# Performance work log

Measured on AMD Instinct MI355X. Metric: run time of the kernel, lower is better.

## Reference

```python
import jax, jax.numpy as jnp
import numpy as np


def _side(x, y, W, w):
    # x: [B, Lx, d] attends over y: [B, Ly, d]
    alpha = jnp.einsum('bld,de->ble', x, W)          # bilinear projection
    alpha = jnp.einsum('ble,bme->blm', alpha, y)     # [B, Lx, Ly]
    alpha = jax.nn.softmax(alpha, axis=1)            # Keras softmax axis=1 (over Lx)
    a = jnp.einsum('blm,bmd->bld', alpha, y)         # attended context [B, Lx, d]
    out = jnp.concatenate([x - a, x * a], axis=-1)   # [B, Lx, 2d]
    beta = jax.nn.softmax(jnp.einsum('ble,eo->blo', out, w)[..., 0], axis=-1)  # [B, Lx]
    return jnp.einsum('bl,ble->be', beta, out)       # pooled [B, 2d]


def setup_inputs() -> dict:
    key = jax.random.key(0)
    k1, k2, k3, k4 = jax.random.split(key, 4)
    B, L, d = 512, 256, 512
    return {
        'i': jax.random.normal(k1, (B, L, d), dtype=jnp.float32),
        'j': jax.random.normal(k2, (B, L, d), dtype=jnp.float32),
        'W': jax.random.normal(k3, (d, d), dtype=jnp.float32) * 0.05,
        'w': jax.random.normal(k4, (2 * d, 1), dtype=jnp.float32) * 0.05,
    }


def reference(i, j, W, w):
    out_i = _side(i, j, W, w)
    out_j = _side(j, i, W, w)
    return (out_i, out_j)
```

## Files before the change

kernel.cpp:

```cpp
#include <hip/hip_runtime.h>

#define LL 256
#define DD 512

typedef _Float16 f16;
typedef _Float16 f16x4_t __attribute__((ext_vector_type(4)));
typedef _Float16 f16x8_t __attribute__((ext_vector_type(8)));
typedef float f32x4_t __attribute__((ext_vector_type(4)));

__device__ __forceinline__ char* swzp(char* base, unsigned row, unsigned byte) {
  return base + (byte ^ ((row & 7u) << 4));
}
__device__ __forceinline__ const char* swzp(const char* base, unsigned row, unsigned byte) {
  return base + (byte ^ ((row & 7u) << 4));
}

__global__ void k_prep(const float* __restrict__ W, f16* __restrict__ Wt) {
  __shared__ float t[64][65];
  int bx = blockIdx.x & 7;
  int by = blockIdx.x >> 3;
  int tx = threadIdx.x & 63, tg = threadIdx.x >> 6;
  for (int r = tg; r < 64; r += 4)
    t[r][tx] = W[(by * 64 + r) * DD + bx * 64 + tx];
  __syncthreads();
  for (int r = tg; r < 64; r += 4)
    Wt[(bx * 64 + r) * DD + by * 64 + tx] = (f16)t[tx][r];
}

struct Smem {
  f16 A_w[256 * 256];
  union {
    struct { f16 bufX[256 * 32]; f16 bufW[128 * 32]; } p0;
    struct { f16 bufP[256 * 32]; f16 bufY[64 * 32]; } pa;
    f16 yT[128 * 64];
  } st;
  float colred[4][64];
  float colmax[64];
  float colinv[64];
  float gp[2][256];
  float beta[256];
};

__global__ __launch_bounds__(512, 2)
void k_main(const float* __restrict__ gi, const float* __restrict__ gj,
            const f16* __restrict__ Wt, const float* __restrict__ wv,
            f16* __restrict__ slabs, float* __restrict__ out) {
  __shared__ Smem sm;
  const int tid = threadIdx.x;
  const int lane = tid & 63;
  const int wave = tid >> 6;
  const int wm = wave & 3, wn = wave >> 2;
  const int lq = lane & 15, lg = lane >> 4;
  const int bid = blockIdx.x;
  const int b = bid >> 1, side = bid & 1;
  const float* __restrict__ x = (side ? gj : gi) + (size_t)b * (LL * DD);
  const float* __restrict__ y = (side ? gi : gj) + (size_t)b * (LL * DD);
  f16* __restrict__ slab = slabs + (size_t)bid * (LL * DD);

  char* const AW = (char*)sm.A_w;
  char* const BX = (char*)sm.st.p0.bufX;
  char* const BW = (char*)sm.st.p0.bufW;
  char* const BP = (char*)sm.st.pa.bufP;
  char* const BY = (char*)sm.st.pa.bufY;
  char* const YT = (char*)sm.st.yT;

  for (int nt = 0; nt < 4; ++nt) {
    f32x4_t acc[4][4];
#pragma unroll
    for (int mf = 0; mf < 4; ++mf)
#pragma unroll
      for (int nf = 0; nf < 4; ++nf)
        acc[mf][nf] = (f32x4_t){0.f, 0.f, 0.f, 0.f};

    for (int kt = 0; kt < 16; ++kt) {
#pragma unroll
      for (int c = tid; c < 1024; c += 512) {
        int row = c >> 2, sl = c & 3;
        const float* src = x + row * DD + kt * 32 + sl * 8;
        float4 a0 = *(const float4*)src;
        float4 a1 = *(const float4*)(src + 4);
        f16x8_t v;
        v[0] = (f16)a0.x; v[1] = (f16)a0.y; v[2] = (f16)a0.z; v[3] = (f16)a0.w;
        v[4] = (f16)a1.x; v[5] = (f16)a1.y; v[6] = (f16)a1.z; v[7] = (f16)a1.w;
        *(f16x8_t*)swzp(BX, row, row * 64u + sl * 16u) = v;
      }
      {
        int row = tid >> 2, sl = tid & 3;
        f16x8_t v = *(const f16x8_t*)(Wt + (nt * 128 + row) * DD + kt * 32 + sl * 8);
        *(f16x8_t*)swzp(BW, row, row * 64u + sl * 16u) = v;
      }
      __syncthreads();
      f16x8_t af[4], bf[4];
#pragma unroll
      for (int mf = 0; mf < 4; ++mf) {
        int row = wm * 64 + mf * 16 + lq;
        af[mf] = *(const f16x8_t*)swzp(BX, row, row * 64u + lg * 16u);
      }
#pragma unroll
      for (int nf = 0; nf < 4; ++nf) {
        int er = wn * 64 + nf * 16 + lq;
        bf[nf] = *(const f16x8_t*)swzp(BW, er, er * 64u + lg * 16u);
      }
#pragma unroll
      for (int mf = 0; mf < 4; ++mf)
#pragma unroll
        for (int nf = 0; nf < 4; ++nf)
          acc[mf][nf] = __builtin_amdgcn_mfma_f32_16x16x32_f16(af[mf], bf[nf], acc[mf][nf], 0, 0, 0);
      __syncthreads();
    }
#pragma unroll
    for (int mf = 0; mf < 4; ++mf)
#pragma unroll
      for (int nf = 0; nf < 4; ++nf)
#pragma unroll
        for (int r = 0; r < 4; ++r) {
          int row = wm * 64 + mf * 16 + lg * 4 + r;
          int col = nt * 128 + wn * 64 + nf * 16 + lq;
          slab[row * DD + col] = (f16)acc[mf][nf][r];
        }
  }
  __threadfence_block();
  __syncthreads();

  for (int mt = 0; mt < 4; ++mt) {
    f32x4_t acc[4][2];
#pragma unroll
    for (int mf = 0; mf < 4; ++mf)
#pragma unroll
      for (int nf = 0; nf < 2; ++nf)
        acc[mf][nf] = (f32x4_t){0.f, 0.f, 0.f, 0.f};

    for (int kt = 0; kt < 16; ++kt) {
#pragma unroll
      for (int c = tid; c < 1024; c += 512) {
        int row = c >> 2, sl = c & 3;
        f16x8_t v = *(const f16x8_t*)(slab + row * DD + kt * 32 + sl * 8);
        *(f16x8_t*)swzp(BP, row, row * 64u + sl * 16u) = v;
      }
      if (tid < 256) {
        int row = tid >> 2, sl = tid & 3;
        const float* src = y + (mt * 64 + row) * DD + kt * 32 + sl * 8;
        float4 a0 = *(const float4*)src;
        float4 a1 = *(const float4*)(src + 4);
        f16x8_t v;
        v[0] = (f16)a0.x; v[1] = (f16)a0.y; v[2] = (f16)a0.z; v[3] = (f16)a0.w;
        v[4] = (f16)a1.x; v[5] = (f16)a1.y; v[6] = (f16)a1.z; v[7] = (f16)a1.w;
        *(f16x8_t*)swzp(BY, row, row * 64u + sl * 16u) = v;
      }
      __syncthreads();
      f16x8_t af[4], bf[2];
#pragma unroll
      for (int mf = 0; mf < 4; ++mf) {
        int row = wm * 64 + mf * 16 + lq;
        af[mf] = *(const f16x8_t*)swzp(BP, row, row * 64u + lg * 16u);
      }
#pragma unroll
      for (int nf = 0; nf < 2; ++nf) {
        int mr = wn * 32 + nf * 16 + lq;
        bf[nf] = *(const f16x8_t*)swzp(BY, mr, mr * 64u + lg * 16u);
      }
#pragma unroll
      for (int mf = 0; mf < 4; ++mf)
#pragma unroll
        for (int nf = 0; nf < 2; ++nf)
          acc[mf][nf] = __builtin_amdgcn_mfma_f32_16x16x32_f16(af[mf], bf[nf], acc[mf][nf], 0, 0, 0);
      __syncthreads();
    }

    float vm[2];
#pragma unroll
    for (int nf = 0; nf < 2; ++nf) {
      float v = -3.4e38f;
#pragma unroll
      for (int mf = 0; mf < 4; ++mf)
#pragma unroll
        for (int r = 0; r < 4; ++r) v = fmaxf(v, acc[mf][nf][r]);
      v = fmaxf(v, __shfl_xor(v, 16));
      v = fmaxf(v, __shfl_xor(v, 32));
      vm[nf] = v;
    }
    if (lane < 16) {
      sm.colred[wm][wn * 32 + lane] = vm[0];
      sm.colred[wm][wn * 32 + 16 + lane] = vm[1];
    }
    __syncthreads();
    if (tid < 64)
      sm.colmax[tid] = fmaxf(fmaxf(sm.colred[0][tid], sm.colred[1][tid]),
                             fmaxf(sm.colred[2][tid], sm.colred[3][tid]));
    __syncthreads();
#pragma unroll
    for (int nf = 0; nf < 2; ++nf) {
      float cm = sm.colmax[wn * 32 + nf * 16 + lq];
      float s = 0.f;
#pragma unroll
      for (int mf = 0; mf < 4; ++mf)
#pragma unroll
        for (int r = 0; r < 4; ++r) {
          float p = __expf(acc[mf][nf][r] - cm);
          acc[mf][nf][r] = p;
          s += p;
        }
      s += __shfl_xor(s, 16);
      s += __shfl_xor(s, 32);
      vm[nf] = s;
    }
    if (lane < 16) {
      sm.colred[wm][wn * 32 + lane] = vm[0];
      sm.colred[wm][wn * 32 + 16 + lane] = vm[1];
    }
    __syncthreads();
    if (tid < 64)
      sm.colinv[tid] = 1.f / (sm.colred[0][tid] + sm.colred[1][tid] +
                              sm.colred[2][tid] + sm.colred[3][tid]);
    __syncthreads();
#pragma unroll
    for (int nf = 0; nf < 2; ++nf) {
      int colg = mt * 64 + wn * 32 + nf * 16 + lq;
      float ci = sm.colinv[wn * 32 + nf * 16 + lq];
#pragma unroll
      for (int mf = 0; mf < 4; ++mf)
#pragma unroll
        for (int r = 0; r < 4; ++r) {
          int row = wm * 64 + mf * 16 + lg * 4 + r;
          *(f16*)swzp(AW, row, row * 512u + colg * 2u) = (f16)(acc[mf][nf][r] * ci);
        }
    }
    __syncthreads();
  }

  float garr[4][4];
#pragma unroll
  for (int mf = 0; mf < 4; ++mf)
#pragma unroll
    for (int r = 0; r < 4; ++r) garr[mf][r] = 0.f;

  for (int dct = 0; dct < 4; ++dct) {
    f32x4_t acc[4][4];
#pragma unroll
    for (int mf = 0; mf < 4; ++mf)
#pragma unroll
      for (int nf = 0; nf < 4; ++nf)
        acc[mf][nf] = (f32x4_t){0.f, 0.f, 0.f, 0.f};

    for (int mh = 0; mh < 4; ++mh) {
      {
        int dc = tid & 127, mq = tid >> 7;
#pragma unroll
        for (int q = 0; q < 4; ++q) {
          int m0 = mq * 16 + q * 4;
          const float* src = y + (size_t)(mh * 64 + m0) * DD + dct * 128 + dc;
          f16x4_t v = {(f16)src[0], (f16)src[DD], (f16)src[2 * DD], (f16)src[3 * DD]};
          *(f16x4_t*)swzp(YT, dc, dc * 128u + m0 * 2u) = v;
        }
      }
      __syncthreads();
#pragma unroll
      for (int ks = 0; ks < 2; ++ks) {
        f16x8_t af[4], bf[4];
#pragma unroll
        for (int mf = 0; mf < 4; ++mf) {
          int row = wm * 64 + mf * 16 + lq;
          af[mf] = *(const f16x8_t*)swzp(AW, row, row * 512u + (mh * 64 + ks * 32 + lg * 8) * 2u);
        }
#pragma unroll
        for (int nf = 0; nf < 4; ++nf) {
          int dcr = wn * 64 + nf * 16 + lq;
          bf[nf] = *(const f16x8_t*)swzp(YT, dcr, dcr * 128u + (ks * 32 + lg * 8) * 2u);
        }
#pragma unroll
        for (int mf = 0; mf < 4; ++mf)
#pragma unroll
          for (int nf = 0; nf < 4; ++nf)
            acc[mf][nf] = __builtin_amdgcn_mfma_f32_16x16x32_f16(af[mf], bf[nf], acc[mf][nf], 0, 0, 0);
      }
      __syncthreads();
    }
#pragma unroll
    for (int mf = 0; mf < 4; ++mf)
#pragma unroll
      for (int r = 0; r < 4; ++r) {
        int row = wm * 64 + mf * 16 + lg * 4 + r;
        float gsum = 0.f;
#pragma unroll
        for (int nf = 0; nf < 4; ++nf) {
          int dc = dct * 128 + wn * 64 + nf * 16 + lq;
          float av = acc[mf][nf][r];
          float xv = x[row * DD + dc];
          gsum += (xv - av) * wv[dc] + (xv * av) * wv[DD + dc];
          slab[row * DD + dc] = (f16)av;
        }
        gsum += __shfl_xor(gsum, 1);
        gsum += __shfl_xor(gsum, 2);
        gsum += __shfl_xor(gsum, 4);
        gsum += __shfl_xor(gsum, 8);
        garr[mf][r] += gsum;
      }
  }
  if (lq == 0) {
#pragma unroll
    for (int mf = 0; mf < 4; ++mf)
#pragma unroll
      for (int r = 0; r < 4; ++r) {
        int row = wm * 64 + mf * 16 + lg * 4 + r;
        sm.gp[wn][row] = garr[mf][r];
      }
  }
  __threadfence_block();
  __syncthreads();

  if (wave == 0) {
    float gv[4];
    float M = -3.4e38f;
#pragma unroll
    for (int q = 0; q < 4; ++q) {
      int l = lane + q * 64;
      gv[q] = sm.gp[0][l] + sm.gp[1][l];
      M = fmaxf(M, gv[q]);
    }
#pragma unroll
    for (int s = 1; s < 64; s <<= 1) M = fmaxf(M, __shfl_xor(M, s));
    float S = 0.f;
    float ev[4];
#pragma unroll
    for (int q = 0; q < 4; ++q) { ev[q] = __expf(gv[q] - M); S += ev[q]; }
#pragma unroll
    for (int s = 1; s < 64; s <<= 1) S += __shfl_xor(S, s);
    float inv = 1.f / S;
#pragma unroll
    for (int q = 0; q < 4; ++q) sm.beta[lane + q * 64] = ev[q] * inv;
  }
  __syncthreads();

  {
    int dc = tid;
    float s1 = 0.f, s2 = 0.f;
    for (int l = 0; l < 256; ++l) {
      float bl = sm.beta[l];
      float av = (float)slab[l * DD + dc];
      float xv = x[l * DD + dc];
      s1 += bl * (xv - av);
      s2 += bl * (xv * av);
    }
    size_t o = (size_t)side * (512u * 1024u) + (size_t)b * 1024u;
    out[o + dc] = s1;
    out[o + DD + dc] = s2;
  }
}

extern "C" void kernel_launch(void* const* d_in, const int* in_sizes, int n_in,
                              void* d_out, int out_size, void* d_ws, size_t ws_size,
                              hipStream_t stream) {
  (void)in_sizes; (void)n_in; (void)out_size; (void)ws_size;
  const float* gi = (const float*)d_in[0];
  const float* gj = (const float*)d_in[1];
  const float* W  = (const float*)d_in[2];
  const float* wv = (const float*)d_in[3];
  float* out = (float*)d_out;
  f16* Wt = (f16*)d_ws;
  f16* slabs = Wt + DD * DD;
  k_prep<<<dim3(64), dim3(256), 0, stream>>>(W, Wt);
  k_main<<<dim3(1024), dim3(512), 0, stream>>>(gi, gj, Wt, wv, slabs, out);
}
```

Measured before the change: 1.148 ms.

## Restructure attention kernel with double-buffered stages, transposed score layout, and block remap

```diff
diff --git a/kernel.cpp b/kernel.cpp
--- a/kernel.cpp
+++ b/kernel.cpp
@@ -8,11 +8,11 @@
 typedef _Float16 f16x8_t __attribute__((ext_vector_type(8)));
 typedef float f32x4_t __attribute__((ext_vector_type(4)));
 
-__device__ __forceinline__ char* swzp(char* base, unsigned row, unsigned byte) {
-  return base + (byte ^ ((row & 7u) << 4));
-}
-__device__ __forceinline__ const char* swzp(const char* base, unsigned row, unsigned byte) {
-  return base + (byte ^ ((row & 7u) << 4));
+__device__ __forceinline__ f16x8_t cvt2(const float4 a, const float4 b) {
+  f16x8_t v;
+  v[0] = (f16)a.x; v[1] = (f16)a.y; v[2] = (f16)a.z; v[3] = (f16)a.w;
+  v[4] = (f16)b.x; v[5] = (f16)b.y; v[6] = (f16)b.z; v[7] = (f16)b.w;
+  return v;
 }
 
 __global__ void k_prep(const float* __restrict__ W, f16* __restrict__ Wt) {
@@ -27,285 +27,389 @@
     Wt[(bx * 64 + r) * DD + by * 64 + tx] = (f16)t[tx][r];
 }
 
-struct Smem {
-  f16 A_w[256 * 256];
-  union {
-    struct { f16 bufX[256 * 32]; f16 bufW[128 * 32]; } p0;
-    struct { f16 bufP[256 * 32]; f16 bufY[64 * 32]; } pa;
-    f16 yT[128 * 64];
-  } st;
-  float colred[4][64];
-  float colmax[64];
-  float colinv[64];
-  float gp[2][256];
-  float beta[256];
-};
 
 __global__ __launch_bounds__(512, 2)
 void k_main(const float* __restrict__ gi, const float* __restrict__ gj,
             const f16* __restrict__ Wt, const float* __restrict__ wv,
             f16* __restrict__ slabs, float* __restrict__ out) {
-  __shared__ Smem sm;
+  __shared__ __align__(16) char R1[131072];
+  __shared__ __align__(16) char R2[16384];
+
   const int tid = threadIdx.x;
   const int lane = tid & 63;
   const int wave = tid >> 6;
-  const int wm = wave & 3, wn = wave >> 2;
   const int lq = lane & 15, lg = lane >> 4;
-  const int bid = blockIdx.x;
-  const int b = bid >> 1, side = bid & 1;
+
+  const int sb = blockIdx.x;
+  const int wk = (sb & 7) * 128 + (sb >> 3);
+  const int b = wk >> 1, side = wk & 1;
   const float* __restrict__ x = (side ? gj : gi) + (size_t)b * (LL * DD);
   const float* __restrict__ y = (side ? gi : gj) + (size_t)b * (LL * DD);
-  f16* __restrict__ slab = slabs + (size_t)bid * (LL * DD);
-
-  char* const AW = (char*)sm.A_w;
-  char* const BX = (char*)sm.st.p0.bufX;
-  char* const BW = (char*)sm.st.p0.bufW;
-  char* const BP = (char*)sm.st.pa.bufP;
-  char* const BY = (char*)sm.st.pa.bufY;
-  char* const YT = (char*)sm.st.yT;
-
-  for (int nt = 0; nt < 4; ++nt) {
-    f32x4_t acc[4][4];
-#pragma unroll
-    for (int mf = 0; mf < 4; ++mf)
-#pragma unroll
-      for (int nf = 0; nf < 4; ++nf)
-        acc[mf][nf] = (f32x4_t){0.f, 0.f, 0.f, 0.f};
-
-    for (int kt = 0; kt < 16; ++kt) {
-#pragma unroll
-      for (int c = tid; c < 1024; c += 512) {
-        int row = c >> 2, sl = c & 3;
-        const float* src = x + row * DD + kt * 32 + sl * 8;
-        float4 a0 = *(const float4*)src;
-        float4 a1 = *(const float4*)(src + 4);
-        f16x8_t v;
-        v[0] = (f16)a0.x; v[1] = (f16)a0.y; v[2] = (f16)a0.z; v[3] = (f16)a0.w;
-        v[4] = (f16)a1.x; v[5] = (f16)a1.y; v[6] = (f16)a1.z; v[7] = (f16)a1.w;
-        *(f16x8_t*)swzp(BX, row, row * 64u + sl * 16u) = v;
-      }
+  f16* __restrict__ slab = slabs + (size_t)wk * (LL * DD);
+
+  char* const R1c = R1;
+  char* const R2c = R2;
+  float* const colred = (float*)R2c;
+  float* const colmax = (float*)(R2c + 2048);
+  float* const colinv = (float*)(R2c + 3072);
+  float* const gp     = (float*)R2c;
+  float* const betas  = (float*)(R2c + 2048);
+
+  {
+    const int wl2 = wave & 1, we4 = wave >> 1;
+    for (int lh = 0; lh < 2; ++lh) {
+      f32x4_t acc[8][4];
+#pragma unroll
+      for (int ef = 0; ef < 8; ++ef)
+#pragma unroll
+        for (int lf = 0; lf < 4; ++lf) acc[ef][lf] = (f32x4_t){0.f, 0.f, 0.f, 0.f};
+
+      const int xrow = tid >> 2;
+      const int xc4 = (tid & 3) * 16;
       {
-        int row = tid >> 2, sl = tid & 3;
-        f16x8_t v = *(const f16x8_t*)(Wt + (nt * 128 + row) * DD + kt * 32 + sl * 8);
-        *(f16x8_t*)swzp(BW, row, row * 64u + sl * 16u) = v;
+        const float* src = x + (size_t)(lh * 128 + xrow) * DD + 0 + xc4;
+        float4 a0 = *(const float4*)src, a1 = *(const float4*)(src + 4);
+        float4 a2 = *(const float4*)(src + 8), a3 = *(const float4*)(src + 12);
+        unsigned swz = (unsigned)(xrow & 7) << 4;
+        *(f16x8_t*)(R1c + xrow * 128 + ((xc4 * 2) ^ swz)) = cvt2(a0, a1);
+        *(f16x8_t*)(R1c + xrow * 128 + ((xc4 * 2 + 16) ^ swz)) = cvt2(a2, a3);
       }
       __syncthreads();
-      f16x8_t af[4], bf[4];
-#pragma unroll
-      for (int mf = 0; mf < 4; ++mf) {
-        int row = wm * 64 + mf * 16 + lq;
-        af[mf] = *(const f16x8_t*)swzp(BX, row, row * 64u + lg * 16u);
-      }
-#pragma unroll
-      for (int nf = 0; nf < 4; ++nf) {
-        int er = wn * 64 + nf * 16 + lq;
-        bf[nf] = *(const f16x8_t*)swzp(BW, er, er * 64u + lg * 16u);
-      }
-#pragma unroll
-      for (int mf = 0; mf < 4; ++mf)
-#pragma unroll
-        for (int nf = 0; nf < 4; ++nf)
-          acc[mf][nf] = __builtin_amdgcn_mfma_f32_16x16x32_f16(af[mf], bf[nf], acc[mf][nf], 0, 0, 0);
-      __syncthreads();
-    }
-#pragma unroll
-    for (int mf = 0; mf < 4; ++mf)
-#pragma unroll
-      for (int nf = 0; nf < 4; ++nf)
-#pragma unroll
-        for (int r = 0; r < 4; ++r) {
-          int row = wm * 64 + mf * 16 + lg * 4 + r;
-          int col = nt * 128 + wn * 64 + nf * 16 + lq;
-          slab[row * DD + col] = (f16)acc[mf][nf][r];
-        }
+
+      for (int s = 0; s < 8; ++s) {
+        char* xbc = R1c + (s & 1) * 16384;
+        char* xbn = R1c + ((s + 1) & 1) * 16384;
+        float4 p0, p1, p2, p3;
+        if (s < 7) {
+          const float* src = x + (size_t)(lh * 128 + xrow) * DD + (s + 1) * 64 + xc4;
+          p0 = *(const float4*)src; p1 = *(const float4*)(src + 4);
+          p2 = *(const float4*)(src + 8); p3 = *(const float4*)(src + 12);
+        }
+#pragma unroll
+        for (int ks = 0; ks < 2; ++ks) {
+          f16x8_t wtF[8], xF[4];
+#pragma unroll
+          for (int ef = 0; ef < 8; ++ef) {
+            int er = we4 * 128 + ef * 16 + lq;
+            wtF[ef] = *(const f16x8_t*)(Wt + (size_t)er * DD + s * 64 + ks * 32 + lg * 8);
+          }
+#pragma unroll
+          for (int lf = 0; lf < 4; ++lf) {
+            int row = wl2 * 64 + lf * 16 + lq;
+            xF[lf] = *(const f16x8_t*)(xbc + row * 128 +
+                       ((ks * 64 + lg * 16) ^ ((unsigned)(row & 7) << 4)));
+          }
+#pragma unroll
+          for (int ef = 0; ef < 8; ++ef)
+#pragma unroll
+            for (int lf = 0; lf < 4; ++lf)
+              acc[ef][lf] = __builtin_amdgcn_mfma_f32_16x16x32_f16(wtF[ef], xF[lf], acc[ef][lf], 0, 0, 0);
+        }
+        if (s < 7) {
+          unsigned swz = (unsigned)(xrow & 7) << 4;
+          *(f16x8_t*)(xbn + xrow * 128 + ((xc4 * 2) ^ swz)) = cvt2(p0, p1);
+          *(f16x8_t*)(xbn + xrow * 128 + ((xc4 * 2 + 16) ^ swz)) = cvt2(p2, p3);
+        }
+        __syncthreads();
+      }
+#pragma unroll
+      for (int ef = 0; ef < 8; ++ef)
+#pragma unroll
+        for (int lf = 0; lf < 4; ++lf) {
+          int l = lh * 128 + wl2 * 64 + lf * 16 + lq;
+          int e = we4 * 128 + ef * 16 + lg * 4;
+          f16x4_t v;
+          v[0] = (f16)acc[ef][lf][0]; v[1] = (f16)acc[ef][lf][1];
+          v[2] = (f16)acc[ef][lf][2]; v[3] = (f16)acc[ef][lf][3];
+          *(f16x4_t*)(slab + (size_t)l * DD + e) = v;
+        }
+    }
   }
-  __threadfence_block();
   __syncthreads();
 
-  for (int mt = 0; mt < 4; ++mt) {
-    f32x4_t acc[4][2];
-#pragma unroll
-    for (int mf = 0; mf < 4; ++mf)
-#pragma unroll
-      for (int nf = 0; nf < 2; ++nf)
-        acc[mf][nf] = (f32x4_t){0.f, 0.f, 0.f, 0.f};
-
-    for (int kt = 0; kt < 16; ++kt) {
-#pragma unroll
-      for (int c = tid; c < 1024; c += 512) {
-        int row = c >> 2, sl = c & 3;
-        f16x8_t v = *(const f16x8_t*)(slab + row * DD + kt * 32 + sl * 8);
-        *(f16x8_t*)swzp(BP, row, row * 64u + sl * 16u) = v;
-      }
-      if (tid < 256) {
-        int row = tid >> 2, sl = tid & 3;
-        const float* src = y + (mt * 64 + row) * DD + kt * 32 + sl * 8;
-        float4 a0 = *(const float4*)src;
-        float4 a1 = *(const float4*)(src + 4);
-        f16x8_t v;
-        v[0] = (f16)a0.x; v[1] = (f16)a0.y; v[2] = (f16)a0.z; v[3] = (f16)a0.w;
-        v[4] = (f16)a1.x; v[5] = (f16)a1.y; v[6] = (f16)a1.z; v[7] = (f16)a1.w;
-        *(f16x8_t*)swzp(BY, row, row * 64u + sl * 16u) = v;
-      }
-      __syncthreads();
-      f16x8_t af[4], bf[2];
-#pragma unroll
-      for (int mf = 0; mf < 4; ++mf) {
-        int row = wm * 64 + mf * 16 + lq;
-        af[mf] = *(const f16x8_t*)swzp(BP, row, row * 64u + lg * 16u);
-      }
-#pragma unroll
-      for (int nf = 0; nf < 2; ++nf) {
-        int mr = wn * 32 + nf * 16 + lq;
-        bf[nf] = *(const f16x8_t*)swzp(BY, mr, mr * 64u + lg * 16u);
-      }
-#pragma unroll
-      for (int mf = 0; mf < 4; ++mf)
-#pragma unroll
-        for (int nf = 0; nf < 2; ++nf)
-          acc[mf][nf] = __builtin_amdgcn_mfma_f32_16x16x32_f16(af[mf], bf[nf], acc[mf][nf], 0, 0, 0);
-      __syncthreads();
-    }
-
-    float vm[2];
-#pragma unroll
-    for (int nf = 0; nf < 2; ++nf) {
-      float v = -3.4e38f;
-#pragma unroll
-      for (int mf = 0; mf < 4; ++mf)
-#pragma unroll
-        for (int r = 0; r < 4; ++r) v = fmaxf(v, acc[mf][nf][r]);
-      v = fmaxf(v, __shfl_xor(v, 16));
-      v = fmaxf(v, __shfl_xor(v, 32));
-      vm[nf] = v;
-    }
-    if (lane < 16) {
-      sm.colred[wm][wn * 32 + lane] = vm[0];
-      sm.colred[wm][wn * 32 + 16 + lane] = vm[1];
-    }
-    __syncthreads();
-    if (tid < 64)
-      sm.colmax[tid] = fmaxf(fmaxf(sm.colred[0][tid], sm.colred[1][tid]),
-                             fmaxf(sm.colred[2][tid], sm.colred[3][tid]));
-    __syncthreads();
-#pragma unroll
-    for (int nf = 0; nf < 2; ++nf) {
-      float cm = sm.colmax[wn * 32 + nf * 16 + lq];
-      float s = 0.f;
-#pragma unroll
-      for (int mf = 0; mf < 4; ++mf)
-#pragma unroll
-        for (int r = 0; r < 4; ++r) {
-          float p = __expf(acc[mf][nf][r] - cm);
-          acc[mf][nf][r] = p;
-          s += p;
-        }
-      s += __shfl_xor(s, 16);
-      s += __shfl_xor(s, 32);
-      vm[nf] = s;
-    }
-    if (lane < 16) {
-      sm.colred[wm][wn * 32 + lane] = vm[0];
-      sm.colred[wm][wn * 32 + 16 + lane] = vm[1];
-    }
-    __syncthreads();
-    if (tid < 64)
-      sm.colinv[tid] = 1.f / (sm.colred[0][tid] + sm.colred[1][tid] +
-                              sm.colred[2][tid] + sm.colred[3][tid]);
-    __syncthreads();
-#pragma unroll
-    for (int nf = 0; nf < 2; ++nf) {
-      int colg = mt * 64 + wn * 32 + nf * 16 + lq;
-      float ci = sm.colinv[wn * 32 + nf * 16 + lq];
-#pragma unroll
-      for (int mf = 0; mf < 4; ++mf)
-#pragma unroll
-        for (int r = 0; r < 4; ++r) {
-          int row = wm * 64 + mf * 16 + lg * 4 + r;
-          *(f16*)swzp(AW, row, row * 512u + colg * 2u) = (f16)(acc[mf][nf][r] * ci);
-        }
-    }
-    __syncthreads();
-  }
-
-  float garr[4][4];
-#pragma unroll
-  for (int mf = 0; mf < 4; ++mf)
-#pragma unroll
-    for (int r = 0; r < 4; ++r) garr[mf][r] = 0.f;
-
-  for (int dct = 0; dct < 4; ++dct) {
-    f32x4_t acc[4][4];
-#pragma unroll
-    for (int mf = 0; mf < 4; ++mf)
-#pragma unroll
-      for (int nf = 0; nf < 4; ++nf)
-        acc[mf][nf] = (f32x4_t){0.f, 0.f, 0.f, 0.f};
-
-    for (int mh = 0; mh < 4; ++mh) {
-      {
-        int dc = tid & 127, mq = tid >> 7;
-#pragma unroll
-        for (int q = 0; q < 4; ++q) {
-          int m0 = mq * 16 + q * 4;
-          const float* src = y + (size_t)(mh * 64 + m0) * DD + dct * 128 + dc;
-          f16x4_t v = {(f16)src[0], (f16)src[DD], (f16)src[2 * DD], (f16)src[3 * DD]};
-          *(f16x4_t*)swzp(YT, dc, dc * 128u + m0 * 2u) = v;
-        }
-      }
-      __syncthreads();
+  {
+    const int wm = wave & 3, wl = wave >> 2;
+    f32x4_t accS[4][8];
+#pragma unroll
+    for (int mf = 0; mf < 4; ++mf)
+#pragma unroll
+      for (int nf = 0; nf < 8; ++nf) accS[mf][nf] = (f32x4_t){0.f, 0.f, 0.f, 0.f};
+
+    const int prow = tid >> 1;
+    const int phalf = tid & 1;
+
+    {
+      unsigned swz = (unsigned)(prow & 7) << 4;
+#pragma unroll
+      for (int q = 0; q < 4; ++q) {
+        f16x8_t pv = *(const f16x8_t*)(slab + (size_t)prow * DD + phalf * 32 + q * 8);
+        *(f16x8_t*)(R1c + prow * 128 + ((phalf * 64 + q * 16) ^ swz)) = pv;
+      }
+      const float* src = y + (size_t)prow * DD + phalf * 32;
+#pragma unroll
+      for (int q = 0; q < 4; ++q) {
+        float4 a0 = *(const float4*)(src + q * 8);
+        float4 a1 = *(const float4*)(src + q * 8 + 4);
+        *(f16x8_t*)(R1c + 65536 + prow * 128 + ((phalf * 64 + q * 16) ^ swz)) = cvt2(a0, a1);
+      }
+    }
+    __syncthreads();
+
+    for (int s = 0; s < 8; ++s) {
+      char* BPc = R1c + (s & 1) * 32768;
+      char* Yc = R1c + 65536 + (s & 1) * 32768;
+      f16x8_t pre_bp[4];
+      float4 pre_y[8];
+      if (s < 7) {
+        int e0n = (s + 1) * 64;
+#pragma unroll
+        for (int q = 0; q < 4; ++q)
+          pre_bp[q] = *(const f16x8_t*)(slab + (size_t)prow * DD + e0n + phalf * 32 + q * 8);
+        const float* src = y + (size_t)prow * DD + e0n + phalf * 32;
+#pragma unroll
+        for (int q = 0; q < 8; ++q) pre_y[q] = *(const float4*)(src + q * 4);
+      }
 #pragma unroll
       for (int ks = 0; ks < 2; ++ks) {
-        f16x8_t af[4], bf[4];
+        f16x8_t aF[4], bF[8];
 #pragma unroll
         for (int mf = 0; mf < 4; ++mf) {
           int row = wm * 64 + mf * 16 + lq;
-          af[mf] = *(const f16x8_t*)swzp(AW, row, row * 512u + (mh * 64 + ks * 32 + lg * 8) * 2u);
-        }
-#pragma unroll
-        for (int nf = 0; nf < 4; ++nf) {
-          int dcr = wn * 64 + nf * 16 + lq;
-          bf[nf] = *(const f16x8_t*)swzp(YT, dcr, dcr * 128u + (ks * 32 + lg * 8) * 2u);
+          aF[mf] = *(const f16x8_t*)(Yc + row * 128 +
+                     ((ks * 64 + lg * 16) ^ ((unsigned)(row & 7) << 4)));
+        }
+#pragma unroll
+        for (int nf = 0; nf < 8; ++nf) {
+          int row = wl * 128 + nf * 16 + lq;
+          bF[nf] = *(const f16x8_t*)(BPc + row * 128 +
+                     ((ks * 64 + lg * 16) ^ ((unsigned)(row & 7) << 4)));
         }
 #pragma unroll
         for (int mf = 0; mf < 4; ++mf)
 #pragma unroll
-          for (int nf = 0; nf < 4; ++nf)
-            acc[mf][nf] = __builtin_amdgcn_mfma_f32_16x16x32_f16(af[mf], bf[nf], acc[mf][nf], 0, 0, 0);
+          for (int nf = 0; nf < 8; ++nf)
+            accS[mf][nf] = __builtin_amdgcn_mfma_f32_16x16x32_f16(aF[mf], bF[nf], accS[mf][nf], 0, 0, 0);
+      }
+      if (s < 7) {
+        char* BPn = R1c + ((s + 1) & 1) * 32768;
+        char* Yn = R1c + 65536 + ((s + 1) & 1) * 32768;
+        unsigned swz = (unsigned)(prow & 7) << 4;
+#pragma unroll
+        for (int q = 0; q < 4; ++q)
+          *(f16x8_t*)(BPn + prow * 128 + ((phalf * 64 + q * 16) ^ swz)) = pre_bp[q];
+#pragma unroll
+        for (int q = 0; q < 4; ++q)
+          *(f16x8_t*)(Yn + prow * 128 + ((phalf * 64 + q * 16) ^ swz)) =
+              cvt2(pre_y[2 * q], pre_y[2 * q + 1]);
       }
       __syncthreads();
     }
+
+    float red[4][4];
 #pragma unroll
     for (int mf = 0; mf < 4; ++mf)
 #pragma unroll
       for (int r = 0; r < 4; ++r) {
-        int row = wm * 64 + mf * 16 + lg * 4 + r;
-        float gsum = 0.f;
-#pragma unroll
-        for (int nf = 0; nf < 4; ++nf) {
-          int dc = dct * 128 + wn * 64 + nf * 16 + lq;
-          float av = acc[mf][nf][r];
-          float xv = x[row * DD + dc];
-          gsum += (xv - av) * wv[dc] + (xv * av) * wv[DD + dc];
-          slab[row * DD + dc] = (f16)av;
-        }
-        gsum += __shfl_xor(gsum, 1);
-        gsum += __shfl_xor(gsum, 2);
-        gsum += __shfl_xor(gsum, 4);
-        gsum += __shfl_xor(gsum, 8);
-        garr[mf][r] += gsum;
+        float v = accS[mf][0][r];
+#pragma unroll
+        for (int nf = 1; nf < 8; ++nf) v = fmaxf(v, accS[mf][nf][r]);
+        v = fmaxf(v, __shfl_xor(v, 1));
+        v = fmaxf(v, __shfl_xor(v, 2));
+        v = fmaxf(v, __shfl_xor(v, 4));
+        v = fmaxf(v, __shfl_xor(v, 8));
+        red[mf][r] = v;
+      }
+    if (lq == 0) {
+#pragma unroll
+      for (int mf = 0; mf < 4; ++mf)
+#pragma unroll
+        for (int r = 0; r < 4; ++r)
+          colred[wl * 256 + wm * 64 + mf * 16 + lg * 4 + r] = red[mf][r];
+    }
+    __syncthreads();
+    if (tid < 256) colmax[tid] = fmaxf(colred[tid], colred[256 + tid]);
+    __syncthreads();
+    float cm[4][4];
+#pragma unroll
+    for (int mf = 0; mf < 4; ++mf)
+#pragma unroll
+      for (int r = 0; r < 4; ++r) cm[mf][r] = colmax[wm * 64 + mf * 16 + lg * 4 + r];
+    __syncthreads();
+#pragma unroll
+    for (int mf = 0; mf < 4; ++mf)
+#pragma unroll
+      for (int r = 0; r < 4; ++r) {
+        float s = 0.f;
+#pragma unroll
+        for (int nf = 0; nf < 8; ++nf) {
+          float p = __expf(accS[mf][nf][r] - cm[mf][r]);
+          accS[mf][nf][r] = p;
+          s += p;
+        }
+        s += __shfl_xor(s, 1);
+        s += __shfl_xor(s, 2);
+        s += __shfl_xor(s, 4);
+        s += __shfl_xor(s, 8);
+        red[mf][r] = s;
+      }
+    if (lq == 0) {
+#pragma unroll
+      for (int mf = 0; mf < 4; ++mf)
+#pragma unroll
+        for (int r = 0; r < 4; ++r)
+          colred[wl * 256 + wm * 64 + mf * 16 + lg * 4 + r] = red[mf][r];
+    }
+    __syncthreads();
+    if (tid < 256) colinv[tid] = 1.f / (colred[tid] + colred[256 + tid]);
+    __syncthreads();
+    float inv[4][4];
+#pragma unroll
+    for (int mf = 0; mf < 4; ++mf)
+#pragma unroll
+      for (int r = 0; r < 4; ++r) inv[mf][r] = colinv[wm * 64 + mf * 16 + lg * 4 + r];
+    __syncthreads();
+#pragma unroll
+    for (int mf = 0; mf < 4; ++mf)
+#pragma unroll
+      for (int nf = 0; nf < 8; ++nf) {
+        int l = wl * 128 + nf * 16 + lq;
+        f16x4_t v;
+        v[0] = (f16)(accS[mf][nf][0] * inv[mf][0]);
+        v[1] = (f16)(accS[mf][nf][1] * inv[mf][1]);
+        v[2] = (f16)(accS[mf][nf][2] * inv[mf][2]);
+        v[3] = (f16)(accS[mf][nf][3] * inv[mf][3]);
+        *(f16x4_t*)(R1c + l * 512 +
+                    ((wm * 128 + mf * 32 + lg * 8) ^ ((unsigned)(l & 7) << 4))) = v;
       }
   }
-  if (lq == 0) {
-#pragma unroll
-    for (int mf = 0; mf < 4; ++mf)
-#pragma unroll
-      for (int r = 0; r < 4; ++r) {
-        int row = wm * 64 + mf * 16 + lg * 4 + r;
-        sm.gp[wn][row] = garr[mf][r];
-      }
+  __syncthreads();
+
+  {
+    const int wl3 = wave & 3, wd = wave >> 2;
+    float garr[4][4];
+#pragma unroll
+    for (int lf = 0; lf < 4; ++lf)
+#pragma unroll
+      for (int r = 0; r < 4; ++r) garr[lf][r] = 0.f;
+
+    const int yd = tid & 127, ymq = tid >> 7;
+    f16* const aT = slab;
+
+    for (int dct = 0; dct < 4; ++dct) {
+      f32x4_t accB[4][4];
+#pragma unroll
+      for (int lf = 0; lf < 4; ++lf)
+#pragma unroll
+        for (int df = 0; df < 4; ++df) accB[lf][df] = (f32x4_t){0.f, 0.f, 0.f, 0.f};
+
+      float lyA[4][4], lyB[4][4];
+#pragma unroll
+      for (int q = 0; q < 4; ++q) {
+        int m0 = ymq * 16 + q * 4;
+#pragma unroll
+        for (int k = 0; k < 4; ++k)
+          lyA[q][k] = y[(size_t)(m0 + k) * DD + dct * 128 + yd];
+      }
+#pragma unroll
+      for (int mh = 0; mh < 4; ++mh) {
+        __syncthreads();
+        {
+          unsigned swz = (unsigned)(yd & 7) << 4;
+#pragma unroll
+          for (int q = 0; q < 4; ++q) {
+            int m0 = ymq * 16 + q * 4;
+            f16x4_t v;
+            if (mh & 1) {
+              v[0] = (f16)lyB[q][0]; v[1] = (f16)lyB[q][1];
+              v[2] = (f16)lyB[q][2]; v[3] = (f16)lyB[q][3];
+            } else {
+              v[0] = (f16)lyA[q][0]; v[1] = (f16)lyA[q][1];
+              v[2] = (f16)lyA[q][2]; v[3] = (f16)lyA[q][3];
+            }
+            *(f16x4_t*)(R2c + yd * 128 + ((m0 * 2) ^ swz)) = v;
+          }
+        }
+        __syncthreads();
+        if (mh < 3) {
+#pragma unroll
+          for (int q = 0; q < 4; ++q) {
+            int m0 = (mh + 1) * 64 + ymq * 16 + q * 4;
+#pragma unroll
+            for (int k = 0; k < 4; ++k) {
+              float lv = y[(size_t)(m0 + k) * DD + dct * 128 + yd];
+              if (mh & 1) lyA[q][k] = lv; else lyB[q][k] = lv;
+            }
+          }
+        }
+#pragma unroll
+        for (int ks = 0; ks < 2; ++ks) {
+          f16x8_t aF[4], bF[4];
+#pragma unroll
+          for (int lf = 0; lf < 4; ++lf) {
+            int row = wl3 * 64 + lf * 16 + lq;
+            aF[lf] = *(const f16x8_t*)(R1c + row * 512 +
+                       ((mh * 128 + ks * 64 + lg * 16) ^ ((unsigned)(row & 7) << 4)));
+          }
+#pragma unroll
+          for (int df = 0; df < 4; ++df) {
+            int row = wd * 64 + df * 16 + lq;
+            bF[df] = *(const f16x8_t*)(R2c + row * 128 +
+                       ((ks * 64 + lg * 16) ^ ((unsigned)(row & 7) << 4)));
+          }
+#pragma unroll
+          for (int lf = 0; lf < 4; ++lf)
+#pragma unroll
+            for (int df = 0; df < 4; ++df)
+              accB[lf][df] = __builtin_amdgcn_mfma_f32_16x16x32_f16(aF[lf], bF[df], accB[lf][df], 0, 0, 0);
+        }
+      }
+      float wvA[4], wvB[4];
+#pragma unroll
+      for (int df = 0; df < 4; ++df) {
+        int d = dct * 128 + wd * 64 + df * 16 + lq;
+        wvA[df] = wv[d];
+        wvB[df] = wv[DD + d];
+      }
+#pragma unroll
+      for (int lf = 0; lf < 4; ++lf)
+#pragma unroll
+        for (int r = 0; r < 4; ++r) {
+          int l = wl3 * 64 + lf * 16 + lg * 4 + r;
+          float gs = 0.f;
+#pragma unroll
+          for (int df = 0; df < 4; ++df) {
+            int d = dct * 128 + wd * 64 + df * 16 + lq;
+            float av = accB[lf][df][r];
+            float xv = x[(size_t)l * DD + d];
+            gs += (xv - av) * wvA[df] + (xv * av) * wvB[df];
+          }
+          gs += __shfl_xor(gs, 1);
+          gs += __shfl_xor(gs, 2);
+          gs += __shfl_xor(gs, 4);
+          gs += __shfl_xor(gs, 8);
+          garr[lf][r] += gs;
+        }
+#pragma unroll
+      for (int lf = 0; lf < 4; ++lf)
+#pragma unroll
+        for (int df = 0; df < 4; ++df) {
+          int d = dct * 128 + wd * 64 + df * 16 + lq;
+          int l0 = wl3 * 64 + lf * 16 + lg * 4;
+          f16x4_t v;
+          v[0] = (f16)accB[lf][df][0]; v[1] = (f16)accB[lf][df][1];
+          v[2] = (f16)accB[lf][df][2]; v[3] = (f16)accB[lf][df][3];
+          *(f16x4_t*)(aT + (size_t)d * LL + l0) = v;
+        }
+    }
+    __syncthreads();
+    if (lq == 0) {
+#pragma unroll
+      for (int lf = 0; lf < 4; ++lf)
+#pragma unroll
+        for (int r = 0; r < 4; ++r)
+          gp[wd * 256 + wl3 * 64 + lf * 16 + lg * 4 + r] = garr[lf][r];
+    }
   }
-  __threadfence_block();
   __syncthreads();
 
   if (wave == 0) {
@@ -314,32 +418,37 @@
 #pragma unroll
     for (int q = 0; q < 4; ++q) {
       int l = lane + q * 64;
-      gv[q] = sm.gp[0][l] + sm.gp[1][l];
+      gv[q] = gp[l] + gp[256 + l];
       M = fmaxf(M, gv[q]);
     }
 #pragma unroll
     for (int s = 1; s < 64; s <<= 1) M = fmaxf(M, __shfl_xor(M, s));
-    float S = 0.f;
-    float ev[4];
+    float S = 0.f, ev[4];
 #pragma unroll
     for (int q = 0; q < 4; ++q) { ev[q] = __expf(gv[q] - M); S += ev[q]; }
 #pragma unroll
     for (int s = 1; s < 64; s <<= 1) S += __shfl_xor(S, s);
     float inv = 1.f / S;
 #pragma unroll
-    for (int q = 0; q < 4; ++q) sm.beta[lane + q * 64] = ev[q] * inv;
+    for (int q = 0; q < 4; ++q) betas[lane + q * 64] = ev[q] * inv;
   }
   __syncthreads();
 
   {
+    const f16* const aT = slab;
     int dc = tid;
     float s1 = 0.f, s2 = 0.f;
-    for (int l = 0; l < 256; ++l) {
-      float bl = sm.beta[l];
-      float av = (float)slab[l * DD + dc];
-      float xv = x[l * DD + dc];
-      s1 += bl * (xv - av);
-      s2 += bl * (xv * av);
+    for (int lb = 0; lb < 32; ++lb) {
+      f16x8_t av8 = *(const f16x8_t*)(aT + (size_t)dc * LL + lb * 8);
+#pragma unroll
+      for (int q = 0; q < 8; ++q) {
+        int l = lb * 8 + q;
+        float bl = betas[l];
+        float av = (float)av8[q];
+        float xv = x[(size_t)l * DD + dc];
+        s1 += bl * (xv - av);
+        s2 += bl * (xv * av);
+      }
     }
     size_t o = (size_t)side * (512u * 1024u) + (size_t)b * 1024u;
     out[o + dc] = s1;
```

After: 1.219 ms. +6.2%, slower.
